# Kernel optimization log

Measured on AMD Instinct MI355X. Metric: run time of the kernel, lower is better.

The kernel has to match this reference:

```python
import jax, jax.numpy as jnp
import numpy as np

INFINITY = 1000000000000000.0


def setup_inputs() -> dict:
    key = jax.random.key(0)
    ks = jax.random.split(key, 6)
    B, Lq, Lk = 8, 256, 256
    Dq, Dk, A = 512, 512, 256
    Q = jax.random.normal(ks[0], (B, Lq, 1, Dq), dtype=jnp.float32)
    K = jax.random.normal(ks[1], (B, 1, Lk, Dk), dtype=jnp.float32)
    mask = jax.random.randint(ks[2], (B, Lq, Lk), 0, 2, dtype=jnp.int32)
    W1 = jax.random.normal(ks[3], (A, Dq), dtype=jnp.float32) / np.sqrt(Dq)
    W2 = jax.random.normal(ks[4], (A, Dk), dtype=jnp.float32) / np.sqrt(Dk)
    w3 = jax.random.normal(ks[5], (A,), dtype=jnp.float32) / np.sqrt(A)
    return {"Q": Q, "K": K, "mask": mask, "W1": W1, "W2": W2, "w3": w3}


def reference(Q, K, mask, W1, W2, w3):
    # Project then broadcast-add: [B,Lq,1,A] + [B,1,Lk,A] -> [B,Lq,Lk,A]
    q_proj = jnp.einsum('blqd,ad->blqa', Q, W1)  # [B,Lq,1,A]
    k_proj = jnp.einsum('bqkd,ad->bqka', K, W2)  # [B,1,Lk,A]
    score = jnp.einsum('blka,a->blk', jnp.tanh(q_proj + k_proj), w3)  # [B,Lq,Lk]
    score = jnp.where(mask == 0, -INFINITY, score)
    return jax.nn.softmax(score, axis=-1)
```

## Files before the change

kernel.cpp:

```cpp
#include <hip/hip_runtime.h>
#include <hip/hip_bf16.h>
#include <cstdint>

constexpr int B  = 8;
constexpr int LQ = 256;
constexpr int LK = 256;
constexpr int D  = 512;
constexpr int A  = 256;

constexpr float NEG_INF   = -1e15f;
constexpr float LOG2E     = 1.4426950408889634f;
constexpr float TWO_LOG2E = 2.8853900817779268f;

constexpr int QP_ELEMS = B * LQ * A;

constexpr int BM  = 64;
constexpr int BN  = 64;
constexpr int BKC = 64;
constexpr int LDK = 72;

typedef short bf16x8 __attribute__((ext_vector_type(8)));
typedef float f32x4  __attribute__((ext_vector_type(4)));

__device__ inline ushort bf16_rne(float x) {
    unsigned u = __float_as_uint(x);
    unsigned r = u + 0x7FFFu + ((u >> 16) & 1u);
    return (ushort)(r >> 16);
}
__device__ inline float bf16_f(ushort h) {
    return __uint_as_float(((unsigned)h) << 16);
}

__device__ inline void stage4(ushort* dh, ushort* dl, float4 v, float s) {
    ushort4 h, l;
    float x;
    x = v.x * s; h.x = bf16_rne(x); l.x = bf16_rne(x - bf16_f(h.x));
    x = v.y * s; h.y = bf16_rne(x); l.y = bf16_rne(x - bf16_f(h.y));
    x = v.z * s; h.z = bf16_rne(x); l.z = bf16_rne(x - bf16_f(h.z));
    x = v.w * s; h.w = bf16_rne(x); l.w = bf16_rne(x - bf16_f(h.w));
    *(ushort4*)dh = h;
    *(ushort4*)dl = l;
}

__global__ __launch_bounds__(256) void proj_gemm(const float* __restrict__ Q,
                                                 const float* __restrict__ Kin,
                                                 const float* __restrict__ W1,
                                                 const float* __restrict__ W2,
                                                 float* __restrict__ qp,
                                                 float* __restrict__ kp) {
    __shared__ ushort LDSB[4][BM][LDK];
    auto* AH = LDSB[0];
    auto* AL = LDSB[1];
    auto* BH = LDSB[2];
    auto* BL = LDSB[3];

    const int t    = threadIdx.x;
    const int lane = t & 63;
    const int wave = t >> 6;
    const int wm   = (wave >> 1) * 32;
    const int wn   = (wave & 1) * 32;
    const int l15  = lane & 15;
    const int lg   = lane >> 4;

    const int tile_n  = blockIdx.x & 3;
    const int tile_m  = blockIdx.x >> 2;
    const int rowbase = tile_m * BM;
    const int cbase   = tile_n * BN;
    const bool isQ    = rowbase < 2048;

    const float* X  = isQ ? (Q + (size_t)rowbase * D)
                          : (Kin + (size_t)(rowbase - 2048) * D);
    const float* Wp = (isQ ? W1 : W2) + (size_t)cbase * D;

    const int sm = t >> 2;
    const int sk = (t & 3) * 16;

    const float* xrow = X + (size_t)sm * D + sk;
    const float* wrow = Wp + (size_t)sm * D + sk;

    f32x4 acc[2][2] = {{{0.f, 0.f, 0.f, 0.f}, {0.f, 0.f, 0.f, 0.f}},
                       {{0.f, 0.f, 0.f, 0.f}, {0.f, 0.f, 0.f, 0.f}}};

    for (int k0 = 0; k0 < D; k0 += BKC) {
        float4 xv0 = *(const float4*)(xrow + k0);
        float4 xv1 = *(const float4*)(xrow + k0 + 4);
        float4 xv2 = *(const float4*)(xrow + k0 + 8);
        float4 xv3 = *(const float4*)(xrow + k0 + 12);
        float4 wv0 = *(const float4*)(wrow + k0);
        float4 wv1 = *(const float4*)(wrow + k0 + 4);
        float4 wv2 = *(const float4*)(wrow + k0 + 8);
        float4 wv3 = *(const float4*)(wrow + k0 + 12);

        __syncthreads();

        stage4(&AH[sm][sk +  0], &AL[sm][sk +  0], xv0, 1.0f);
        stage4(&AH[sm][sk +  4], &AL[sm][sk +  4], xv1, 1.0f);
        stage4(&AH[sm][sk +  8], &AL[sm][sk +  8], xv2, 1.0f);
        stage4(&AH[sm][sk + 12], &AL[sm][sk + 12], xv3, 1.0f);
        stage4(&BH[sm][sk +  0], &BL[sm][sk +  0], wv0, TWO_LOG2E);
        stage4(&BH[sm][sk +  4], &BL[sm][sk +  4], wv1, TWO_LOG2E);
        stage4(&BH[sm][sk +  8], &BL[sm][sk +  8], wv2, TWO_LOG2E);
        stage4(&BH[sm][sk + 12], &BL[sm][sk + 12], wv3, TWO_LOG2E);

        __syncthreads();

#pragma unroll
        for (int ks = 0; ks < BKC; ks += 32) {
            const int kf = ks + lg * 8;
            bf16x8 ah0 = *(const bf16x8*)&AH[wm + l15][kf];
            bf16x8 ah1 = *(const bf16x8*)&AH[wm + 16 + l15][kf];
            bf16x8 al0 = *(const bf16x8*)&AL[wm + l15][kf];
            bf16x8 al1 = *(const bf16x8*)&AL[wm + 16 + l15][kf];
            bf16x8 bh0 = *(const bf16x8*)&BH[wn + l15][kf];
            bf16x8 bh1 = *(const bf16x8*)&BH[wn + 16 + l15][kf];
            bf16x8 bl0 = *(const bf16x8*)&BL[wn + l15][kf];
            bf16x8 bl1 = *(const bf16x8*)&BL[wn + 16 + l15][kf];

            acc[0][0] = __builtin_amdgcn_mfma_f32_16x16x32_bf16(ah0, bh0, acc[0][0], 0, 0, 0);
            acc[0][1] = __builtin_amdgcn_mfma_f32_16x16x32_bf16(ah0, bh1, acc[0][1], 0, 0, 0);
            acc[1][0] = __builtin_amdgcn_mfma_f32_16x16x32_bf16(ah1, bh0, acc[1][0], 0, 0, 0);
            acc[1][1] = __builtin_amdgcn_mfma_f32_16x16x32_bf16(ah1, bh1, acc[1][1], 0, 0, 0);

            acc[0][0] = __builtin_amdgcn_mfma_f32_16x16x32_bf16(ah0, bl0, acc[0][0], 0, 0, 0);
            acc[0][1] = __builtin_amdgcn_mfma_f32_16x16x32_bf16(ah0, bl1, acc[0][1], 0, 0, 0);
            acc[1][0] = __builtin_amdgcn_mfma_f32_16x16x32_bf16(ah1, bl0, acc[1][0], 0, 0, 0);
            acc[1][1] = __builtin_amdgcn_mfma_f32_16x16x32_bf16(ah1, bl1, acc[1][1], 0, 0, 0);

            acc[0][0] = __builtin_amdgcn_mfma_f32_16x16x32_bf16(al0, bh0, acc[0][0], 0, 0, 0);
            acc[0][1] = __builtin_amdgcn_mfma_f32_16x16x32_bf16(al0, bh1, acc[0][1], 0, 0, 0);
            acc[1][0] = __builtin_amdgcn_mfma_f32_16x16x32_bf16(al1, bh0, acc[1][0], 0, 0, 0);
            acc[1][1] = __builtin_amdgcn_mfma_f32_16x16x32_bf16(al1, bh1, acc[1][1], 0, 0, 0);
        }
    }

    float ex[2][2][4];
#pragma unroll
    for (int mi = 0; mi < 2; ++mi)
#pragma unroll
        for (int ni = 0; ni < 2; ++ni)
#pragma unroll
            for (int r = 0; r < 4; ++r)
                ex[mi][ni][r] = __builtin_amdgcn_exp2f(acc[mi][ni][r]);

    if (isQ) {
#pragma unroll
        for (int mi = 0; mi < 2; ++mi)
#pragma unroll
            for (int ni = 0; ni < 2; ++ni)
#pragma unroll
                for (int r = 0; r < 4; ++r) {
                    int row = rowbase + wm + mi * 16 + lg * 4 + r;
                    int col = cbase + wn + ni * 16 + l15;
                    qp[(size_t)row * A + col] = ex[mi][ni][r];
                }
    } else {
        __syncthreads();
        float* T = (float*)&LDSB[0][0][0];
#pragma unroll
        for (int mi = 0; mi < 2; ++mi)
#pragma unroll
            for (int ni = 0; ni < 2; ++ni)
#pragma unroll
                for (int r = 0; r < 4; ++r) {
                    int m = wm + mi * 16 + lg * 4 + r;
                    int n = wn + ni * 16 + l15;
                    T[m * 65 + n] = ex[mi][ni][r];
                }
        __syncthreads();

        const int bb    = (rowbase - 2048) >> 8;
        const int kbase = rowbase & 255;
        float* dstb = kp + (size_t)bb * A * LK;
#pragma unroll
        for (int j = 0; j < 16; ++j) {
            int g  = j * 256 + t;
            int ii = g & 1;
            int kk = (g >> 1) & 63;
            int p  = g >> 7;
            dstb[((size_t)(cbase / 2 + p) * LK + kbase + kk) * 2 + ii] =
                T[kk * 65 + 2 * p + ii];
        }
    }
}

__global__ __launch_bounds__(256) void score_softmax(const float* __restrict__ qp,
                                                     const float* __restrict__ kpT,
                                                     const int* __restrict__ mask,
                                                     const float* __restrict__ w3,
                                                     float* __restrict__ out) {
    const int t    = threadIdx.x;
    const int row0 = blockIdx.x * 4;
    const int b    = row0 >> 8;

    const float* kpb = kpT + (size_t)b * A * LK;
    const float* q0  = qp + (size_t)row0 * A;

    float acc0 = 0.f, acc1 = 0.f, acc2 = 0.f, acc3 = 0.f;

#pragma unroll 4
    for (int a = 0; a < A; a += 2) {
        float2 ek = *(const float2*)(kpb + ((size_t)(a >> 1) * LK + t) * 2);
        float w0  = w3[a], w1 = w3[a + 1];
        float q0a = q0[a],         q0b = q0[a + 1];
        float q1a = q0[A + a],     q1b = q0[A + a + 1];
        float q2a = q0[2 * A + a], q2b = q0[2 * A + a + 1];
        float q3a = q0[3 * A + a], q3b = q0[3 * A + a + 1];

        float f0 = 1.0f + q0a * ek.x;
        float f1 = 1.0f + q1a * ek.x;
        float f2 = 1.0f + q2a * ek.x;
        float f3 = 1.0f + q3a * ek.x;
        float rA = __builtin_amdgcn_rcpf(f0 * f1);
        float rB = __builtin_amdgcn_rcpf(f2 * f3);
        acc0 = fmaf(f1 * rA, w0, acc0);
        acc1 = fmaf(f0 * rA, w0, acc1);
        acc2 = fmaf(f3 * rB, w0, acc2);
        acc3 = fmaf(f2 * rB, w0, acc3);

        float g0 = 1.0f + q0b * ek.y;
        float g1 = 1.0f + q1b * ek.y;
        float g2 = 1.0f + q2b * ek.y;
        float g3 = 1.0f + q3b * ek.y;
        float rC = __builtin_amdgcn_rcpf(g0 * g1);
        float rD = __builtin_amdgcn_rcpf(g2 * g3);
        acc0 = fmaf(g1 * rC, w1, acc0);
        acc1 = fmaf(g0 * rC, w1, acc1);
        acc2 = fmaf(g3 * rD, w1, acc2);
        acc3 = fmaf(g2 * rD, w1, acc3);
    }

    const int* mrow = mask + (size_t)row0 * LK;
    float sc0 = (mrow[t]          == 0) ? NEG_INF : -2.0f * acc0;
    float sc1 = (mrow[LK + t]     == 0) ? NEG_INF : -2.0f * acc1;
    float sc2 = (mrow[2 * LK + t] == 0) ? NEG_INF : -2.0f * acc2;
    float sc3 = (mrow[3 * LK + t] == 0) ? NEG_INF : -2.0f * acc3;

    __shared__ float red[4][8];
    const int wave = t >> 6, lane = t & 63;

    float m0 = sc0, m1 = sc1, m2 = sc2, m3 = sc3;
#pragma unroll
    for (int off = 32; off > 0; off >>= 1) {
        m0 = fmaxf(m0, __shfl_xor(m0, off));
        m1 = fmaxf(m1, __shfl_xor(m1, off));
        m2 = fmaxf(m2, __shfl_xor(m2, off));
        m3 = fmaxf(m3, __shfl_xor(m3, off));
    }
    if (lane == 0) {
        red[0][wave] = m0; red[1][wave] = m1;
        red[2][wave] = m2; red[3][wave] = m3;
    }
    __syncthreads();
    float rmax0 = fmaxf(fmaxf(red[0][0], red[0][1]), fmaxf(red[0][2], red[0][3]));
    float rmax1 = fmaxf(fmaxf(red[1][0], red[1][1]), fmaxf(red[1][2], red[1][3]));
    float rmax2 = fmaxf(fmaxf(red[2][0], red[2][1]), fmaxf(red[2][2], red[2][3]));
    float rmax3 = fmaxf(fmaxf(red[3][0], red[3][1]), fmaxf(red[3][2], red[3][3]));
    __syncthreads();

    float p0 = __builtin_amdgcn_exp2f((sc0 - rmax0) * LOG2E);
    float p1 = __builtin_amdgcn_exp2f((sc1 - rmax1) * LOG2E);
    float p2 = __builtin_amdgcn_exp2f((sc2 - rmax2) * LOG2E);
    float p3 = __builtin_amdgcn_exp2f((sc3 - rmax3) * LOG2E);

    float s0 = p0, s1 = p1, s2 = p2, s3 = p3;
#pragma unroll
    for (int off = 32; off > 0; off >>= 1) {
        s0 += __shfl_xor(s0, off);
        s1 += __shfl_xor(s1, off);
        s2 += __shfl_xor(s2, off);
        s3 += __shfl_xor(s3, off);
    }
    if (lane == 0) {
        red[0][wave] = s0; red[1][wave] = s1;
        red[2][wave] = s2; red[3][wave] = s3;
    }
    __syncthreads();
    float sum0 = (red[0][0] + red[0][1]) + (red[0][2] + red[0][3]);
    float sum1 = (red[1][0] + red[1][1]) + (red[1][2] + red[1][3]);
    float sum2 = (red[2][0] + red[2][1]) + (red[2][2] + red[2][3]);
    float sum3 = (red[3][0] + red[3][1]) + (red[3][2] + red[3][3]);

    out[(size_t)row0 * LK + t]       = p0 * __builtin_amdgcn_rcpf(sum0);
    out[(size_t)(row0 + 1) * LK + t] = p1 * __builtin_amdgcn_rcpf(sum1);
    out[(size_t)(row0 + 2) * LK + t] = p2 * __builtin_amdgcn_rcpf(sum2);
    out[(size_t)(row0 + 3) * LK + t] = p3 * __builtin_amdgcn_rcpf(sum3);
}

extern "C" void kernel_launch(void* const* d_in, const int* in_sizes, int n_in,
                              void* d_out, int out_size, void* d_ws, size_t ws_size,
                              hipStream_t stream) {
    const float* Q    = (const float*)d_in[0];
    const float* K    = (const float*)d_in[1];
    const int*   mask = (const int*)d_in[2];
    const float* W1   = (const float*)d_in[3];
    const float* W2   = (const float*)d_in[4];
    const float* w3   = (const float*)d_in[5];
    float* out = (float*)d_out;

    float* ws  = (float*)d_ws;
    float* qp  = ws;
    float* kpT = ws + QP_ELEMS;

    proj_gemm<<<256, 256, 0, stream>>>(Q, K, W1, W2, qp, kpT);
    score_softmax<<<(B * LQ) / 4, 256, 0, stream>>>(qp, kpT, mask, w3, out);
}
```

Baseline: 42.39 us.

## Halve projection GEMM N-tile to double grid and simplify bf16 split

The projection GEMM tile width along the attention dimension goes from 64 to 32, so the grid doubles from 256 to 512 blocks and more CUs are occupied on the MI355X. The hi/lo bf16 split now truncates instead of rounding-to-nearest, packs pairs into uint4 for wider LDS stores, and the 2*log2e scale is moved from the W operand into the epilogue. Each block now redoes the X-tile load and conversion for half as many outputs, which adds redundant global traffic. Truncating the hi part changes the numerics slightly, though the lo correction term still compensates for most of the error.

```diff
diff --git a/kernel.cpp b/kernel.cpp
--- a/kernel.cpp
+++ b/kernel.cpp
@@ -15,31 +15,27 @@
 constexpr int QP_ELEMS = B * LQ * A;
 
 constexpr int BM  = 64;
-constexpr int BN  = 64;
+constexpr int BN  = 32;
 constexpr int BKC = 64;
 constexpr int LDK = 72;
 
 typedef short bf16x8 __attribute__((ext_vector_type(8)));
 typedef float f32x4  __attribute__((ext_vector_type(4)));
 
-__device__ inline ushort bf16_rne(float x) {
-    unsigned u = __float_as_uint(x);
-    unsigned r = u + 0x7FFFu + ((u >> 16) & 1u);
-    return (ushort)(r >> 16);
-}
-__device__ inline float bf16_f(ushort h) {
-    return __uint_as_float(((unsigned)h) << 16);
-}
-
-__device__ inline void stage4(ushort* dh, ushort* dl, float4 v, float s) {
-    ushort4 h, l;
-    float x;
-    x = v.x * s; h.x = bf16_rne(x); l.x = bf16_rne(x - bf16_f(h.x));
-    x = v.y * s; h.y = bf16_rne(x); l.y = bf16_rne(x - bf16_f(h.y));
-    x = v.z * s; h.z = bf16_rne(x); l.z = bf16_rne(x - bf16_f(h.z));
-    x = v.w * s; h.w = bf16_rne(x); l.w = bf16_rne(x - bf16_f(h.w));
-    *(ushort4*)dh = h;
-    *(ushort4*)dl = l;
+__device__ inline void split2(float x0, float x1, unsigned& hi, unsigned& lo) {
+    unsigned u0 = __float_as_uint(x0), u1 = __float_as_uint(x1);
+    unsigned h0 = u0 & 0xFFFF0000u, h1 = u1 & 0xFFFF0000u;
+    hi = h1 | (u0 >> 16);
+    float l0 = x0 - __uint_as_float(h0);
+    float l1 = x1 - __uint_as_float(h1);
+    lo = (__float_as_uint(l1) & 0xFFFF0000u) | (__float_as_uint(l0) >> 16);
+}
+
+__device__ inline void cvt8(float4 a, float4 b, uint4& hi, uint4& lo) {
+    split2(a.x, a.y, hi.x, lo.x);
+    split2(a.z, a.w, hi.y, lo.y);
+    split2(b.x, b.y, hi.z, lo.z);
+    split2(b.z, b.w, hi.w, lo.w);
 }
 
 __global__ __launch_bounds__(256) void proj_gemm(const float* __restrict__ Q,
@@ -48,22 +44,19 @@
                                                  const float* __restrict__ W2,
                                                  float* __restrict__ qp,
                                                  float* __restrict__ kp) {
-    __shared__ ushort LDSB[4][BM][LDK];
-    auto* AH = LDSB[0];
-    auto* AL = LDSB[1];
-    auto* BH = LDSB[2];
-    auto* BL = LDSB[3];
+    __shared__ ushort AH[BM][LDK], AL[BM][LDK];
+    __shared__ ushort BH[BN][LDK], BL[BN][LDK];
 
     const int t    = threadIdx.x;
     const int lane = t & 63;
     const int wave = t >> 6;
     const int wm   = (wave >> 1) * 32;
-    const int wn   = (wave & 1) * 32;
+    const int wn   = (wave & 1) * 16;
     const int l15  = lane & 15;
     const int lg   = lane >> 4;
 
-    const int tile_n  = blockIdx.x & 3;
-    const int tile_m  = blockIdx.x >> 2;
+    const int tile_n  = blockIdx.x & 7;
+    const int tile_m  = blockIdx.x >> 3;
     const int rowbase = tile_m * BM;
     const int cbase   = tile_n * BN;
     const bool isQ    = rowbase < 2048;
@@ -72,14 +65,15 @@
                           : (Kin + (size_t)(rowbase - 2048) * D);
     const float* Wp = (isQ ? W1 : W2) + (size_t)cbase * D;
 
-    const int sm = t >> 2;
-    const int sk = (t & 3) * 16;
-
-    const float* xrow = X + (size_t)sm * D + sk;
-    const float* wrow = Wp + (size_t)sm * D + sk;
-
-    f32x4 acc[2][2] = {{{0.f, 0.f, 0.f, 0.f}, {0.f, 0.f, 0.f, 0.f}},
-                       {{0.f, 0.f, 0.f, 0.f}, {0.f, 0.f, 0.f, 0.f}}};
+    const int sxm = t >> 2;
+    const int sxk = (t & 3) * 16;
+    const int swm = t >> 3;
+    const int swk = (t & 7) * 8;
+
+    const float* xrow = X + (size_t)sxm * D + sxk;
+    const float* wrow = Wp + (size_t)swm * D + swk;
+
+    f32x4 acc[2] = {{0.f, 0.f, 0.f, 0.f}, {0.f, 0.f, 0.f, 0.f}};
 
     for (int k0 = 0; k0 < D; k0 += BKC) {
         float4 xv0 = *(const float4*)(xrow + k0);
@@ -88,19 +82,21 @@
         float4 xv3 = *(const float4*)(xrow + k0 + 12);
         float4 wv0 = *(const float4*)(wrow + k0);
         float4 wv1 = *(const float4*)(wrow + k0 + 4);
-        float4 wv2 = *(const float4*)(wrow + k0 + 8);
-        float4 wv3 = *(const float4*)(wrow + k0 + 12);
-
-        __syncthreads();
-
-        stage4(&AH[sm][sk +  0], &AL[sm][sk +  0], xv0, 1.0f);
-        stage4(&AH[sm][sk +  4], &AL[sm][sk +  4], xv1, 1.0f);
-        stage4(&AH[sm][sk +  8], &AL[sm][sk +  8], xv2, 1.0f);
-        stage4(&AH[sm][sk + 12], &AL[sm][sk + 12], xv3, 1.0f);
-        stage4(&BH[sm][sk +  0], &BL[sm][sk +  0], wv0, TWO_LOG2E);
-        stage4(&BH[sm][sk +  4], &BL[sm][sk +  4], wv1, TWO_LOG2E);
-        stage4(&BH[sm][sk +  8], &BL[sm][sk +  8], wv2, TWO_LOG2E);
-        stage4(&BH[sm][sk + 12], &BL[sm][sk + 12], wv3, TWO_LOG2E);
+
+        __syncthreads();
+
+        uint4 h0, l0, h1, l1;
+        cvt8(xv0, xv1, h0, l0);
+        cvt8(xv2, xv3, h1, l1);
+        *(uint4*)&AH[sxm][sxk]     = h0;
+        *(uint4*)&AH[sxm][sxk + 8] = h1;
+        *(uint4*)&AL[sxm][sxk]     = l0;
+        *(uint4*)&AL[sxm][sxk + 8] = l1;
+
+        uint4 hw, lw;
+        cvt8(wv0, wv1, hw, lw);
+        *(uint4*)&BH[swm][swk] = hw;
+        *(uint4*)&BL[swm][swk] = lw;
 
         __syncthreads();
 
@@ -111,74 +107,58 @@
             bf16x8 ah1 = *(const bf16x8*)&AH[wm + 16 + l15][kf];
             bf16x8 al0 = *(const bf16x8*)&AL[wm + l15][kf];
             bf16x8 al1 = *(const bf16x8*)&AL[wm + 16 + l15][kf];
-            bf16x8 bh0 = *(const bf16x8*)&BH[wn + l15][kf];
-            bf16x8 bh1 = *(const bf16x8*)&BH[wn + 16 + l15][kf];
-            bf16x8 bl0 = *(const bf16x8*)&BL[wn + l15][kf];
-            bf16x8 bl1 = *(const bf16x8*)&BL[wn + 16 + l15][kf];
-
-            acc[0][0] = __builtin_amdgcn_mfma_f32_16x16x32_bf16(ah0, bh0, acc[0][0], 0, 0, 0);
-            acc[0][1] = __builtin_amdgcn_mfma_f32_16x16x32_bf16(ah0, bh1, acc[0][1], 0, 0, 0);
-            acc[1][0] = __builtin_amdgcn_mfma_f32_16x16x32_bf16(ah1, bh0, acc[1][0], 0, 0, 0);
-            acc[1][1] = __builtin_amdgcn_mfma_f32_16x16x32_bf16(ah1, bh1, acc[1][1], 0, 0, 0);
-
-            acc[0][0] = __builtin_amdgcn_mfma_f32_16x16x32_bf16(ah0, bl0, acc[0][0], 0, 0, 0);
-            acc[0][1] = __builtin_amdgcn_mfma_f32_16x16x32_bf16(ah0, bl1, acc[0][1], 0, 0, 0);
-            acc[1][0] = __builtin_amdgcn_mfma_f32_16x16x32_bf16(ah1, bl0, acc[1][0], 0, 0, 0);
-            acc[1][1] = __builtin_amdgcn_mfma_f32_16x16x32_bf16(ah1, bl1, acc[1][1], 0, 0, 0);
-
-            acc[0][0] = __builtin_amdgcn_mfma_f32_16x16x32_bf16(al0, bh0, acc[0][0], 0, 0, 0);
-            acc[0][1] = __builtin_amdgcn_mfma_f32_16x16x32_bf16(al0, bh1, acc[0][1], 0, 0, 0);
-            acc[1][0] = __builtin_amdgcn_mfma_f32_16x16x32_bf16(al1, bh0, acc[1][0], 0, 0, 0);
-            acc[1][1] = __builtin_amdgcn_mfma_f32_16x16x32_bf16(al1, bh1, acc[1][1], 0, 0, 0);
+            bf16x8 bh  = *(const bf16x8*)&BH[wn + l15][kf];
+            bf16x8 bl  = *(const bf16x8*)&BL[wn + l15][kf];
+
+            acc[0] = __builtin_amdgcn_mfma_f32_16x16x32_bf16(ah0, bh, acc[0], 0, 0, 0);
+            acc[1] = __builtin_amdgcn_mfma_f32_16x16x32_bf16(ah1, bh, acc[1], 0, 0, 0);
+            acc[0] = __builtin_amdgcn_mfma_f32_16x16x32_bf16(ah0, bl, acc[0], 0, 0, 0);
+            acc[1] = __builtin_amdgcn_mfma_f32_16x16x32_bf16(ah1, bl, acc[1], 0, 0, 0);
+            acc[0] = __builtin_amdgcn_mfma_f32_16x16x32_bf16(al0, bh, acc[0], 0, 0, 0);
+            acc[1] = __builtin_amdgcn_mfma_f32_16x16x32_bf16(al1, bh, acc[1], 0, 0, 0);
         }
     }
 
-    float ex[2][2][4];
+    float ex[2][4];
 #pragma unroll
     for (int mi = 0; mi < 2; ++mi)
 #pragma unroll
-        for (int ni = 0; ni < 2; ++ni)
-#pragma unroll
-            for (int r = 0; r < 4; ++r)
-                ex[mi][ni][r] = __builtin_amdgcn_exp2f(acc[mi][ni][r]);
+        for (int r = 0; r < 4; ++r)
+            ex[mi][r] = __builtin_amdgcn_exp2f(acc[mi][r] * TWO_LOG2E);
 
     if (isQ) {
 #pragma unroll
         for (int mi = 0; mi < 2; ++mi)
 #pragma unroll
-            for (int ni = 0; ni < 2; ++ni)
-#pragma unroll
-                for (int r = 0; r < 4; ++r) {
-                    int row = rowbase + wm + mi * 16 + lg * 4 + r;
-                    int col = cbase + wn + ni * 16 + l15;
-                    qp[(size_t)row * A + col] = ex[mi][ni][r];
-                }
+            for (int r = 0; r < 4; ++r) {
+                int row = rowbase + wm + mi * 16 + lg * 4 + r;
+                int col = cbase + wn + l15;
+                qp[(size_t)row * A + col] = ex[mi][r];
+            }
     } else {
         __syncthreads();
-        float* T = (float*)&LDSB[0][0][0];
+        float* T = (float*)&AH[0][0];
 #pragma unroll
         for (int mi = 0; mi < 2; ++mi)
 #pragma unroll
-            for (int ni = 0; ni < 2; ++ni)
-#pragma unroll
-                for (int r = 0; r < 4; ++r) {
-                    int m = wm + mi * 16 + lg * 4 + r;
-                    int n = wn + ni * 16 + l15;
-                    T[m * 65 + n] = ex[mi][ni][r];
-                }
+            for (int r = 0; r < 4; ++r) {
+                int m = wm + mi * 16 + lg * 4 + r;
+                int n = wn + l15;
+                T[m * 33 + n] = ex[mi][r];
+            }
         __syncthreads();
 
         const int bb    = (rowbase - 2048) >> 8;
         const int kbase = rowbase & 255;
         float* dstb = kp + (size_t)bb * A * LK;
 #pragma unroll
-        for (int j = 0; j < 16; ++j) {
+        for (int j = 0; j < 8; ++j) {
             int g  = j * 256 + t;
             int ii = g & 1;
             int kk = (g >> 1) & 63;
             int p  = g >> 7;
-            dstb[((size_t)(cbase / 2 + p) * LK + kbase + kk) * 2 + ii] =
-                T[kk * 65 + 2 * p + ii];
+            dstb[((size_t)(tile_n * 16 + p) * LK + kbase + kk) * 2 + ii] =
+                T[kk * 33 + 2 * p + ii];
         }
     }
 }
@@ -301,6 +281,6 @@
     float* qp  = ws;
     float* kpT = ws + QP_ELEMS;
 
-    proj_gemm<<<256, 256, 0, stream>>>(Q, K, W1, W2, qp, kpT);
+    proj_gemm<<<512, 256, 0, stream>>>(Q, K, W1, W2, qp, kpT);
     score_softmax<<<(B * LQ) / 4, 256, 0, stream>>>(qp, kpT, mask, w3, out);
 }
```

Result: faster. 39.28 us (median of 2 runs) (-7.4%).
